# Optimization experiments

Hardware: AMD Instinct MI355X
Metric: run time of the kernel (lower is better)

The kernel has to match this reference:

```python
import math
import jax, jax.numpy as jnp
import numpy as np

NH, NKV, HD, THETA = 32, 8, 128, 500000.0

def rotate_half(x):
    x1, x2 = jnp.split(x, 2, axis=-1)
    return jnp.concatenate((-x2, x1), axis=-1)

def rope_cos_sin(seq_len, dim, base, dtype):
    inv_freq = 1.0 / (base ** (jnp.arange(0, dim, 2, dtype=jnp.float32) / dim))
    t = jnp.arange(seq_len, dtype=jnp.float32)
    freqs = jnp.outer(t, inv_freq)              # [S, dim/2]
    emb = jnp.concatenate((freqs, freqs), -1)   # [S, dim]
    return jnp.cos(emb).astype(dtype), jnp.sin(emb).astype(dtype)

def setup_inputs() -> dict:
    key = jax.random.key(0)
    ks = jax.random.split(key, 5)
    B, S, H = 1, 2048, 4096
    sc = 1.0 / math.sqrt(H)
    return {
        'x':  jax.random.normal(ks[0], (B, S, H), jnp.float32),
        'wq': jax.random.normal(ks[1], (H, H), jnp.float32) * sc,
        'wk': jax.random.normal(ks[2], (NKV * HD, H), jnp.float32) * sc,
        'wv': jax.random.normal(ks[3], (NKV * HD, H), jnp.float32) * sc,
        'wo': jax.random.normal(ks[4], (H, H), jnp.float32) * sc,
    }

def attention(x, wq, wk, wv, wo):
    B, S, H = x.shape
    n_rep = NH // NKV
    q = (x @ wq.T).reshape(B, S, NH, HD).transpose(0, 2, 1, 3)    # [B,NH,S,HD]
    k = (x @ wk.T).reshape(B, S, NKV, HD).transpose(0, 2, 1, 3)   # [B,NKV,S,HD]
    v = (x @ wv.T).reshape(B, S, NKV, HD).transpose(0, 2, 1, 3)
    cos, sin = rope_cos_sin(S, HD, THETA, x.dtype)                # [S,HD]
    cos = cos[None, None]; sin = sin[None, None]
    q = q * cos + rotate_half(q) * sin
    k = k * cos + rotate_half(k) * sin
    k = jnp.repeat(k, n_rep, axis=1)                               # [B,NH,S,HD]
    v = jnp.repeat(v, n_rep, axis=1)
    scores = jnp.einsum('bhqd,bhkd->bhqk', q, k) / math.sqrt(HD)
    causal = jnp.tril(jnp.ones((S, S), dtype=bool))
    scores = jnp.where(causal, scores, jnp.finfo(scores.dtype).min)
    probs = jax.nn.softmax(scores, axis=-1)
    out = jnp.einsum('bhqk,bhkd->bhqd', probs, v)                  # [B,NH,S,HD]
    out = out.transpose(0, 2, 1, 3).reshape(B, S, H)
    return out @ wo.T

def reference(x, wq, wk, wv, wo):
    return attention(x, wq, wk, wv, wo)
```

## Files before the change

### kernel.cpp

```cpp
#include <hip/hip_runtime.h>
#include <hip/hip_bf16.h>
#include <math.h>

typedef __bf16 bf16x8 __attribute__((ext_vector_type(8)));
typedef __bf16 bf16x4 __attribute__((ext_vector_type(4)));
typedef unsigned short u16x8 __attribute__((ext_vector_type(8)));
typedef float  f32x4  __attribute__((ext_vector_type(4)));

constexpr int kS   = 2048;
constexpr int kH   = 4096;
constexpr int kNH  = 32;
constexpr int kNKV = 8;
constexpr int kHD  = 128;
constexpr int kQKV = kH + 2 * kNKV * kHD;
constexpr int kKOff = kH;
constexpr int kVOff = kH + kNKV * kHD;

__global__ void cast_bf16(const float* __restrict__ in, __bf16* __restrict__ out, int n4) {
    int i = blockIdx.x * blockDim.x + threadIdx.x;
    if (i < n4) {
        float4 f = ((const float4*)in)[i];
        bf16x4 o;
        o[0] = (__bf16)f.x; o[1] = (__bf16)f.y; o[2] = (__bf16)f.z; o[3] = (__bf16)f.w;
        ((bf16x4*)out)[i] = o;
    }
}

__global__ void cast_all(const float* __restrict__ x, const float* __restrict__ wq,
                         const float* __restrict__ wk, const float* __restrict__ wv,
                         __bf16* __restrict__ xb, __bf16* __restrict__ wqkv) {
    int i = blockIdx.x * 256 + threadIdx.x;
    float4 f;
    __bf16* dst;
    int di;
    if (i < (1 << 21)) {
        f = ((const float4*)x)[i];
        dst = xb; di = i;
    } else {
        int j = i - (1 << 21);
        const float4* s = (j < (1 << 22)) ? ((const float4*)wq + j)
                        : (j < (5 << 20)) ? ((const float4*)wk + (j - (1 << 22)))
                                          : ((const float4*)wv + (j - (5 << 20)));
        f = *s;
        dst = wqkv; di = j;
    }
    bf16x4 o;
    o[0] = (__bf16)f.x; o[1] = (__bf16)f.y; o[2] = (__bf16)f.z; o[3] = (__bf16)f.w;
    ((bf16x4*)dst)[di] = o;
}

constexpr int BM = 128, BN = 128, BK = 64;

__device__ inline void gld16(const __bf16* g, __bf16* l) {
    __builtin_amdgcn_global_load_lds((const __attribute__((address_space(1))) void*)g,
                                     (__attribute__((address_space(3))) void*)l, 16, 0, 0);
}

template <typename OutT>
__global__ __launch_bounds__(256) void gemm_nt(const __bf16* __restrict__ A,
                                               const __bf16* __restrict__ B,
                                               OutT* __restrict__ C,
                                               int M, int N, int K) {
    __shared__ __align__(16) __bf16 As[BM * BK];
    __shared__ __align__(16) __bf16 Bs[BN * BK];
    const int tid  = threadIdx.x;
    const int w    = tid >> 6, lane = tid & 63;
    const int m0   = blockIdx.y * BM, n0 = blockIdx.x * BN;
    const int wm   = (w >> 1) * 64, wn = (w & 1) * 64;
    const int lr   = lane & 15, g8 = lane >> 4;

    const int l3 = lane >> 3;
    const int lc = (lane & 7) ^ l3;
    const __bf16 *gA[4], *gB[4];
    __bf16 *lA[4], *lB[4];
#pragma unroll
    for (int c = 0; c < 4; c++) {
        int G = w * 4 + c;
        gA[c] = A + (size_t)(m0 + G * 8 + l3) * K + lc * 8;
        gB[c] = B + (size_t)(n0 + G * 8 + l3) * K + lc * 8;
        lA[c] = As + G * 512;
        lB[c] = Bs + G * 512;
    }

    f32x4 acc[4][4];
#pragma unroll
    for (int i = 0; i < 4; i++)
#pragma unroll
        for (int j = 0; j < 4; j++) acc[i][j] = (f32x4)(0.f);

    for (int k0 = 0; k0 < K; k0 += BK) {
#pragma unroll
        for (int c = 0; c < 4; c++) {
            gld16(gA[c] + k0, lA[c]);
            gld16(gB[c] + k0, lB[c]);
        }
        __syncthreads();

        const int rx = lr & 7;
#pragma unroll
        for (int kc = 0; kc < 2; kc++) {
            bf16x8 af[4], bfr[4];
#pragma unroll
            for (int i = 0; i < 4; i++)
                af[i]  = *(const bf16x8*)&As[(wm + i * 16 + lr) * BK + (((kc * 4 + g8) ^ rx) * 8)];
#pragma unroll
            for (int j = 0; j < 4; j++)
                bfr[j] = *(const bf16x8*)&Bs[(wn + j * 16 + lr) * BK + (((kc * 4 + g8) ^ rx) * 8)];
#pragma unroll
            for (int i = 0; i < 4; i++)
#pragma unroll
                for (int j = 0; j < 4; j++)
                    acc[i][j] = __builtin_amdgcn_mfma_f32_16x16x32_bf16(af[i], bfr[j], acc[i][j], 0, 0, 0);
        }
        __syncthreads();
    }

    const int cr = g8 * 4, cc = lr;
#pragma unroll
    for (int i = 0; i < 4; i++)
#pragma unroll
        for (int j = 0; j < 4; j++) {
            OutT* Cp = C + (size_t)(m0 + wm + i * 16 + cr) * N + (n0 + wn + j * 16 + cc);
#pragma unroll
            for (int r = 0; r < 4; r++) Cp[(size_t)r * N] = (OutT)acc[i][j][r];
        }
}

__global__ void rope_qkv(__bf16* __restrict__ qkv) {
    int idx  = blockIdx.x * 256 + threadIdx.x;
    int d    = idx & 63;
    int rest = idx >> 6;
    int hh   = rest % (kNH + kNKV);
    int s    = rest / (kNH + kNKV);
    float inv_freq = powf(500000.0f, -(float)d * (1.0f / 64.0f));
    float sn, cs;
    sincosf((float)s * inv_freq, &sn, &cs);
    __bf16* base = qkv + (size_t)s * kQKV + ((hh < kNH) ? hh * kHD : kKOff + (hh - kNH) * kHD);
    float sc = (hh < kNH) ? 0.088388347648318447f : 1.0f;
    float a = (float)base[d], b = (float)base[d + 64];
    base[d]      = (__bf16)((a * cs - b * sn) * sc);
    base[d + 64] = (__bf16)((b * cs + a * sn) * sc);
}

constexpr int VTP = 72;

__global__ __launch_bounds__(256) void flash_attn(const __bf16* __restrict__ qkv,
                                                  __bf16* __restrict__ ob) {
    __shared__ __align__(16) __bf16 Ks[64 * 128];
    __shared__ __align__(16) __bf16 Vt[128 * VTP];
    __shared__ __align__(16) __bf16 Ps[4 * 16 * 64];

    const int tid  = threadIdx.x;
    const int wave = tid >> 6, lane = tid & 63;
    const int bx   = blockIdx.x;
    const int kvh  = bx & 7;
    const int qt   = 127 - (bx >> 3);
    const int h    = kvh * 4 + wave;
    const int r    = lane & 15, g = lane >> 4;
    const int r7   = r & 7;
    const int qglob = qt * 16 + r;

    __bf16* Pw = Ps + wave * 16 * 64;
    const __bf16* kbase = qkv + kKOff + kvh * kHD;
    const __bf16* vbase = qkv + kVOff + kvh * kHD;

    int krow[4], kgc[4];
#pragma unroll
    for (int c = 0; c < 4; c++) {
        krow[c] = wave * 16 + c * 4 + (lane >> 4);
        kgc[c]  = (lane & 15) ^ (krow[c] & 15);
    }

    bf16x8 qfrag[4];
    const __bf16* qrow = qkv + (size_t)(qt * 16 + r) * kQKV + h * kHD + g * 8;
#pragma unroll
    for (int c = 0; c < 4; c++) qfrag[c] = *(const bf16x8*)(qrow + c * 32);

    f32x4 o[8];
#pragma unroll
    for (int dt = 0; dt < 8; dt++) o[dt] = (f32x4)(0.f);
    float mrow = -3.0e38f, lrow = 0.f;

    const int nkt = qt / 4 + 1;
    for (int kt = 0; kt < nkt; ++kt) {
#pragma unroll
        for (int c = 0; c < 4; c++)
            gld16(kbase + (size_t)(kt * 64 + krow[c]) * kQKV + kgc[c] * 8,
                  Ks + (wave * 4 + c) * 512);
#pragma unroll
        for (int i = 0; i < 2; i++) {
            int task = i * 256 + tid;
            int p = task & 31, c = task >> 5;
            const __bf16* v0 = vbase + (size_t)(kt * 64 + 2 * p) * kQKV + c * 8;
            u16x8 a = __builtin_bit_cast(u16x8, *(const bf16x8*)v0);
            u16x8 b = __builtin_bit_cast(u16x8, *(const bf16x8*)(v0 + kQKV));
#pragma unroll
            for (int j = 0; j < 8; j++) {
                unsigned int pk = (unsigned int)a[j] | ((unsigned int)b[j] << 16);
                *(unsigned int*)(Vt + (c * 8 + j) * VTP + 2 * p) = pk;
            }
        }
        __syncthreads();

        f32x4 st[4];
#pragma unroll
        for (int t = 0; t < 4; t++) st[t] = (f32x4)(0.f);
#pragma unroll
        for (int c = 0; c < 4; c++) {
#pragma unroll
            for (int t = 0; t < 4; t++) {
                bf16x8 kf = *(const bf16x8*)&Ks[(t * 16 + r) * 128 + (((c * 4 + g) ^ r) * 8)];
                st[t] = __builtin_amdgcn_mfma_f32_16x16x32_bf16(kf, qfrag[c], st[t], 0, 0, 0);
            }
        }

        if (kt == nkt - 1) {
#pragma unroll
            for (int t = 0; t < 4; t++)
#pragma unroll
                for (int reg = 0; reg < 4; reg++) {
                    int key = kt * 64 + t * 16 + g * 4 + reg;
                    if (key > qglob) st[t][reg] = -3.0e38f;
                }
        }

        float mloc = -3.0e38f;
#pragma unroll
        for (int t = 0; t < 4; t++)
#pragma unroll
            for (int reg = 0; reg < 4; reg++) mloc = fmaxf(mloc, st[t][reg]);
        mloc = fmaxf(mloc, __shfl_xor(mloc, 16));
        mloc = fmaxf(mloc, __shfl_xor(mloc, 32));
        float mnew  = fmaxf(mrow, mloc);
        float alpha = __expf(mrow - mnew);
        mrow = mnew;
        float lsum = 0.f;
#pragma unroll
        for (int t = 0; t < 4; t++)
#pragma unroll
            for (int reg = 0; reg < 4; reg++) {
                float pv = __expf(st[t][reg] - mnew);
                st[t][reg] = pv;
                lsum += pv;
            }
        lsum += __shfl_xor(lsum, 16);
        lsum += __shfl_xor(lsum, 32);
        lrow = lrow * alpha + lsum;

        float ar[4];
#pragma unroll
        for (int reg = 0; reg < 4; reg++) ar[reg] = __shfl(alpha, g * 4 + reg);
#pragma unroll
        for (int dt = 0; dt < 8; dt++)
#pragma unroll
            for (int reg = 0; reg < 4; reg++) o[dt][reg] *= ar[reg];

#pragma unroll
        for (int t = 0; t < 4; t++) {
            bf16x4 pb;
#pragma unroll
            for (int j = 0; j < 4; j++) pb[j] = (__bf16)st[t][j];
            int p8 = t * 4 + g;
            *(bf16x4*)&Pw[r * 64 + (((p8 >> 1) ^ r7) * 8) + ((p8 & 1) * 4)] = pb;
        }
        __asm__ volatile("s_waitcnt lgkmcnt(0)" ::: "memory");

#pragma unroll
        for (int kc = 0; kc < 2; kc++) {
            bf16x8 pf = *(const bf16x8*)&Pw[r * 64 + (((kc * 4 + g) ^ r7) * 8)];
#pragma unroll
            for (int dt = 0; dt < 8; dt++) {
                bf16x8 vf = *(const bf16x8*)&Vt[(dt * 16 + r) * VTP + kc * 32 + g * 8];
                o[dt] = __builtin_amdgcn_mfma_f32_16x16x32_bf16(pf, vf, o[dt], 0, 0, 0);
            }
        }
        __syncthreads();
    }

    float linv = 1.f / lrow;
    float lr4[4];
#pragma unroll
    for (int reg = 0; reg < 4; reg++) lr4[reg] = __shfl(linv, g * 4 + reg);
#pragma unroll
    for (int dt = 0; dt < 8; dt++)
#pragma unroll
        for (int reg = 0; reg < 4; reg++) {
            int qq = g * 4 + reg, dd = dt * 16 + r;
            ob[(size_t)(qt * 16 + qq) * kH + h * kHD + dd] = (__bf16)(o[dt][reg] * lr4[reg]);
        }
}

extern "C" void kernel_launch(void* const* d_in, const int* in_sizes, int n_in,
                              void* d_out, int out_size, void* d_ws, size_t ws_size,
                              hipStream_t stream) {
    const float* x  = (const float*)d_in[0];
    const float* wq = (const float*)d_in[1];
    const float* wk = (const float*)d_in[2];
    const float* wv = (const float*)d_in[3];
    const float* wo = (const float*)d_in[4];
    float* out = (float*)d_out;

    char* p = (char*)d_ws;
    auto alloc = [&](size_t bytes) {
        char* r = p;
        p += (bytes + 255) & ~(size_t)255;
        return r;
    };
    __bf16* xb    = (__bf16*)alloc((size_t)kS * kH * 2);
    __bf16* wqkvb = (__bf16*)alloc((size_t)kQKV * kH * 2);
    __bf16* qkv   = (__bf16*)alloc((size_t)kS * kQKV * 2);
    __bf16* ao    = xb;
    __bf16* wob   = wqkvb;

    cast_all<<<dim3(1 << 15), 256, 0, stream>>>(x, wq, wk, wv, xb, wqkvb);

    gemm_nt<__bf16><<<dim3(kQKV / BN, kS / BM), 256, 0, stream>>>(xb, wqkvb, qkv, kS, kQKV, kH);

    rope_qkv<<<dim3(kS * (kNH + kNKV) * 64 / 256), 256, 0, stream>>>(qkv);

    cast_bf16<<<dim3((kH * kH / 4) / 256), 256, 0, stream>>>(wo, wob, kH * kH / 4);

    flash_attn<<<dim3(kNKV * (kS / 16)), 256, 0, stream>>>(qkv, ao);

    gemm_nt<float><<<dim3(kH / BN, kS / BM), 256, 0, stream>>>(ao, wob, out, kS, kH, kH);
}
```

Measured before the change: 516.9 us.

## Replace GEMM with 8-wave triple-buffered pipelined kernel and vectorize RoPE

Replaces the 128x128 single-buffered GEMM with a 512-thread kernel using 256-wide (or 128x256) tiles, a BK of 32, and triple-buffered LDS. Global-to-LDS loads are issued two stages ahead, with explicit vmcnt waits, split barriers and s_setprio around the MFMA blocks, and the workgroup id is remapped for L2 locality. The aim is to hide memory latency and reduce barrier stalls in the QKV and output projections. RoPE is vectorized to 8 elements per thread, and the angle is computed with exp2 plus a fractional-revolution reduction and fast sin/cos, which costs some precision in exchange for less transcendental work.

```diff
diff --git a/kernel.cpp b/kernel.cpp
--- a/kernel.cpp
+++ b/kernel.cpp
@@ -49,75 +49,138 @@
     ((bf16x4*)dst)[di] = o;
 }
 
-constexpr int BM = 128, BN = 128, BK = 64;
-
 __device__ inline void gld16(const __bf16* g, __bf16* l) {
     __builtin_amdgcn_global_load_lds((const __attribute__((address_space(1))) void*)g,
                                      (__attribute__((address_space(3))) void*)l, 16, 0, 0);
 }
 
-template <typename OutT>
-__global__ __launch_bounds__(256) void gemm_nt(const __bf16* __restrict__ A,
-                                               const __bf16* __restrict__ B,
-                                               OutT* __restrict__ C,
-                                               int M, int N, int K) {
-    __shared__ __align__(16) __bf16 As[BM * BK];
-    __shared__ __align__(16) __bf16 Bs[BN * BK];
-    const int tid  = threadIdx.x;
-    const int w    = tid >> 6, lane = tid & 63;
-    const int m0   = blockIdx.y * BM, n0 = blockIdx.x * BN;
-    const int wm   = (w >> 1) * 64, wn = (w & 1) * 64;
-    const int lr   = lane & 15, g8 = lane >> 4;
-
-    const int l3 = lane >> 3;
-    const int lc = (lane & 7) ^ l3;
-    const __bf16 *gA[4], *gB[4];
-    __bf16 *lA[4], *lB[4];
-#pragma unroll
-    for (int c = 0; c < 4; c++) {
-        int G = w * 4 + c;
-        gA[c] = A + (size_t)(m0 + G * 8 + l3) * K + lc * 8;
-        gB[c] = B + (size_t)(n0 + G * 8 + l3) * K + lc * 8;
-        lA[c] = As + G * 512;
-        lB[c] = Bs + G * 512;
-    }
-
-    f32x4 acc[4][4];
-#pragma unroll
-    for (int i = 0; i < 4; i++)
+constexpr int GBK = 32, GBN = 256;
+
+template <typename OutT, int GBM>
+__global__ __launch_bounds__(512, 2) void gemm8(const __bf16* __restrict__ A,
+                                                const __bf16* __restrict__ B,
+                                                OutT* __restrict__ C,
+                                                int M, int N, int K, int nbx) {
+    static_assert(GBM == 256 || GBM == 128, "");
+    constexpr int PH  = GBM / 128;
+    constexpr int FM  = GBM / 32;
+    constexpr int AG  = GBM / 128;
+    constexpr int BG  = 2;
+    constexpr int GPK = AG + BG;
+    constexpr int ASZ = GBM * GBK;
+    constexpr int BSZ = GBN * GBK;
+
+    __shared__ __align__(16) __bf16 Ab[3][ASZ];
+    __shared__ __align__(16) __bf16 Bb[3][BSZ];
+
+    const int tid = threadIdx.x, w = tid >> 6, lane = tid & 63;
+    const int lr = lane & 15, g = lane >> 4;
+
+    const int nwg = (int)gridDim.x;
+    const int bid = (int)blockIdx.x;
+    const int id2 = (bid & 7) * (nwg >> 3) + (bid >> 3);
+    const int m0 = (id2 / nbx) * GBM, n0 = (id2 % nbx) * GBN;
+
+    const int wm = (w >> 2) * (GBM / 2), wn = (w & 3) * 64;
+
+    const __bf16* ga[AG]; int la[AG];
+    const __bf16* gb[BG]; int lb[BG];
+#pragma unroll
+    for (int a = 0; a < AG; a++) {
+        int G = a * 512 + tid, row = G >> 2;
+        int lg = (G & 3) ^ ((row >> 1) & 3);
+        ga[a] = A + (size_t)(m0 + row) * K + lg * 8;
+        la[a] = G * 8;
+    }
+#pragma unroll
+    for (int b = 0; b < BG; b++) {
+        int G = b * 512 + tid, row = G >> 2;
+        int lg = (G & 3) ^ ((row >> 1) & 3);
+        gb[b] = B + (size_t)(n0 + row) * K + lg * 8;
+        lb[b] = G * 8;
+    }
+
+    int pao[FM], pbo[4];
+    const int sw = (lr >> 1) & 3;
+#pragma unroll
+    for (int i = 0; i < FM; i++) pao[i] = (wm + i * 16 + lr) * GBK + ((g ^ sw) * 8);
+#pragma unroll
+    for (int j = 0; j < 4; j++)  pbo[j] = (wn + j * 16 + lr) * GBK + ((g ^ sw) * 8);
+
+    f32x4 acc[FM][4];
+#pragma unroll
+    for (int i = 0; i < FM; i++)
 #pragma unroll
         for (int j = 0; j < 4; j++) acc[i][j] = (f32x4)(0.f);
 
-    for (int k0 = 0; k0 < K; k0 += BK) {
-#pragma unroll
-        for (int c = 0; c < 4; c++) {
-            gld16(gA[c] + k0, lA[c]);
-            gld16(gB[c] + k0, lB[c]);
-        }
-        __syncthreads();
-
-        const int rx = lr & 7;
-#pragma unroll
-        for (int kc = 0; kc < 2; kc++) {
+    const int NT = K / GBK;
+
+#pragma unroll
+    for (int z = 0; z < 2; z++) {
+#pragma unroll
+        for (int a = 0; a < AG; a++) gld16(ga[a] + z * GBK, &Ab[z][la[a]]);
+#pragma unroll
+        for (int b = 0; b < BG; b++) gld16(gb[b] + z * GBK, &Bb[z][lb[b]]);
+    }
+    if constexpr (GPK == 4) asm volatile("s_waitcnt vmcnt(4)" ::: "memory");
+    else                    asm volatile("s_waitcnt vmcnt(3)" ::: "memory");
+    __builtin_amdgcn_s_barrier();
+
+    int q = 0;
+    for (int Z = 0; Z < NT; ++Z) {
+        const int qs = (q + 2 >= 3) ? q - 1 : q + 2;
+        const bool stg = Z < NT - 2;
+#pragma unroll
+        for (int p = 0; p < PH; p++) {
             bf16x8 af[4], bfr[4];
 #pragma unroll
+            for (int i = 0; i < 4; i++) af[i]  = *(const bf16x8*)&Ab[q][pao[p * 4 + i]];
+#pragma unroll
+            for (int j = 0; j < 4; j++) bfr[j] = *(const bf16x8*)&Bb[q][pbo[j]];
+
+            if (stg) {
+                if constexpr (PH == 2) {
+                    if (p == 0) {
+#pragma unroll
+                        for (int a = 0; a < AG; a++) gld16(ga[a] + (Z + 2) * GBK, &Ab[qs][la[a]]);
+                    } else {
+#pragma unroll
+                        for (int b = 0; b < BG; b++) gld16(gb[b] + (Z + 2) * GBK, &Bb[qs][lb[b]]);
+                    }
+                } else {
+#pragma unroll
+                    for (int a = 0; a < AG; a++) gld16(ga[a] + (Z + 2) * GBK, &Ab[qs][la[a]]);
+#pragma unroll
+                    for (int b = 0; b < BG; b++) gld16(gb[b] + (Z + 2) * GBK, &Bb[qs][lb[b]]);
+                }
+            }
+
+            __builtin_amdgcn_s_barrier();
+            __builtin_amdgcn_s_setprio(1);
+#pragma unroll
             for (int i = 0; i < 4; i++)
-                af[i]  = *(const bf16x8*)&As[(wm + i * 16 + lr) * BK + (((kc * 4 + g8) ^ rx) * 8)];
-#pragma unroll
-            for (int j = 0; j < 4; j++)
-                bfr[j] = *(const bf16x8*)&Bs[(wn + j * 16 + lr) * BK + (((kc * 4 + g8) ^ rx) * 8)];
-#pragma unroll
-            for (int i = 0; i < 4; i++)
 #pragma unroll
                 for (int j = 0; j < 4; j++)
-                    acc[i][j] = __builtin_amdgcn_mfma_f32_16x16x32_bf16(af[i], bfr[j], acc[i][j], 0, 0, 0);
-        }
-        __syncthreads();
-    }
-
-    const int cr = g8 * 4, cc = lr;
-#pragma unroll
-    for (int i = 0; i < 4; i++)
+                    acc[p * 4 + i][j] = __builtin_amdgcn_mfma_f32_16x16x32_bf16(
+                        af[i], bfr[j], acc[p * 4 + i][j], 0, 0, 0);
+            __builtin_amdgcn_s_setprio(0);
+
+            if (p == PH - 1) {
+                if (Z < NT - 2) {
+                    if constexpr (GPK == 4) asm volatile("s_waitcnt vmcnt(4)" ::: "memory");
+                    else                    asm volatile("s_waitcnt vmcnt(3)" ::: "memory");
+                } else if (Z == NT - 2) {
+                    asm volatile("s_waitcnt vmcnt(0)" ::: "memory");
+                }
+            }
+            __builtin_amdgcn_s_barrier();
+        }
+        q = (q + 1 == 3) ? 0 : q + 1;
+    }
+
+    const int cr = g * 4, cc = lr;
+#pragma unroll
+    for (int i = 0; i < FM; i++)
 #pragma unroll
         for (int j = 0; j < 4; j++) {
             OutT* Cp = C + (size_t)(m0 + wm + i * 16 + cr) * N + (n0 + wn + j * 16 + cc);
@@ -128,18 +191,28 @@
 
 __global__ void rope_qkv(__bf16* __restrict__ qkv) {
     int idx  = blockIdx.x * 256 + threadIdx.x;
-    int d    = idx & 63;
-    int rest = idx >> 6;
+    int d8   = idx & 7;
+    int rest = idx >> 3;
     int hh   = rest % (kNH + kNKV);
     int s    = rest / (kNH + kNKV);
-    float inv_freq = powf(500000.0f, -(float)d * (1.0f / 64.0f));
-    float sn, cs;
-    sincosf((float)s * inv_freq, &sn, &cs);
     __bf16* base = qkv + (size_t)s * kQKV + ((hh < kNH) ? hh * kHD : kKOff + (hh - kNH) * kHD);
     float sc = (hh < kNH) ? 0.088388347648318447f : 1.0f;
-    float a = (float)base[d], b = (float)base[d + 64];
-    base[d]      = (__bf16)((a * cs - b * sn) * sc);
-    base[d + 64] = (__bf16)((b * cs + a * sn) * sc);
+    bf16x8 va = *(const bf16x8*)(base + d8 * 8);
+    bf16x8 vb = *(const bf16x8*)(base + 64 + d8 * 8);
+    bf16x8 ra, rb;
+#pragma unroll
+    for (int j = 0; j < 8; j++) {
+        int d = d8 * 8 + j;
+        float rev = (float)s * exp2f(fmaf((float)d, -0.2958057589f, -2.6514961295f));
+        rev -= floorf(rev);
+        float ang = rev * 6.28318530718f;
+        float sn = __sinf(ang), cs = __cosf(ang);
+        float a = (float)va[j], b = (float)vb[j];
+        ra[j] = (__bf16)((a * cs - b * sn) * sc);
+        rb[j] = (__bf16)((b * cs + a * sn) * sc);
+    }
+    *(bf16x8*)(base + d8 * 8)      = ra;
+    *(bf16x8*)(base + 64 + d8 * 8) = rb;
 }
 
 constexpr int VTP = 72;
@@ -314,13 +387,15 @@
 
     cast_all<<<dim3(1 << 15), 256, 0, stream>>>(x, wq, wk, wv, xb, wqkvb);
 
-    gemm_nt<__bf16><<<dim3(kQKV / BN, kS / BM), 256, 0, stream>>>(xb, wqkvb, qkv, kS, kQKV, kH);
-
-    rope_qkv<<<dim3(kS * (kNH + kNKV) * 64 / 256), 256, 0, stream>>>(qkv);
+    gemm8<__bf16, 256><<<dim3((kQKV / GBN) * (kS / 256)), 512, 0, stream>>>(
+        xb, wqkvb, qkv, kS, kQKV, kH, kQKV / GBN);
+
+    rope_qkv<<<dim3(kS * (kNH + kNKV) * 8 / 256), 256, 0, stream>>>(qkv);
 
     cast_bf16<<<dim3((kH * kH / 4) / 256), 256, 0, stream>>>(wo, wob, kH * kH / 4);
 
     flash_attn<<<dim3(kNKV * (kS / 16)), 256, 0, stream>>>(qkv, ao);
 
-    gemm_nt<float><<<dim3(kH / BN, kS / BM), 256, 0, stream>>>(ao, wob, out, kS, kH, kH);
-}
+    gemm8<float, 128><<<dim3((kH / GBN) * (kS / 128)), 512, 0, stream>>>(
+        ao, wob, out, kS, kH, kH, kH / GBN);
+}
```

Result: faster. 496.3 us (-4.0%).
